# Kernel tuning notes

Hardware: AMD Instinct MI355X
Metric: run time of the kernel (lower is better)

## Reference

```python
import jax, jax.numpy as jnp
import numpy as np

N, F, E, T = 50000, 128, 800000, 8


def setup_inputs() -> dict:
    key = jax.random.key(0)
    ks = jax.random.split(key, 10)
    s = 1.0 / np.sqrt(F)
    return {
        "x": jax.random.normal(ks[0], (N, F), jnp.float32),
        "edge_index": jax.random.randint(ks[1], (2, E), 0, N, jnp.int64),
        "edge_weight": jax.random.uniform(ks[2], (E,), jnp.float32),
        "W0": jax.random.normal(ks[3], (F, F), jnp.float32) * s,
        "Wih": jax.random.normal(ks[4], (3 * F, F), jnp.float32) * s,
        "Whh": jax.random.normal(ks[5], (3 * F, F), jnp.float32) * s,
        "bih": jax.random.normal(ks[6], (3 * F,), jnp.float32) * s,
        "bhh": jax.random.normal(ks[7], (3 * F,), jnp.float32) * s,
        "Wlin": jax.random.normal(ks[8], (T, F), jnp.float32) * s,
        "blin": jax.random.normal(ks[9], (T,), jnp.float32) * s,
    }


def _evolve_weight(W0, Wih, Whh, bih, bhh):
    # One GRU step with input = hidden = W0 (rows of weight matrix as batch).
    gi = W0 @ Wih.T + bih  # [F, 3F]
    gh = W0 @ Whh.T + bhh
    ir, iz, inn = jnp.split(gi, 3, axis=1)
    hr, hz, hn = jnp.split(gh, 3, axis=1)
    r = jax.nn.sigmoid(ir + hr)
    z = jax.nn.sigmoid(iz + hz)
    n = jnp.tanh(inn + r * hn)
    return (1.0 - z) * n + z * W0  # [F, F]


def reference(x, edge_index, edge_weight, W0, Wih, Whh, bih, bhh, Wlin, blin):
    n_nodes = x.shape[0]
    W = _evolve_weight(W0, Wih, Whh, bih, bhh)
    # gcn_norm with added self-loops (fill value 1.0), symmetric normalization
    loop = jnp.arange(n_nodes, dtype=edge_index.dtype)
    row = jnp.concatenate([edge_index[0], loop])
    col = jnp.concatenate([edge_index[1], loop])
    ew = jnp.concatenate([edge_weight, jnp.ones((n_nodes,), edge_weight.dtype)])
    deg = jax.ops.segment_sum(ew, col, num_segments=n_nodes)
    dinv = jnp.where(deg > 0, jax.lax.rsqrt(jnp.where(deg > 0, deg, 1.0)), 0.0)
    norm = dinv[row] * ew * dinv[col]  # [E+N]
    xw = x @ W  # [N, F]
    h = jax.ops.segment_sum(norm[:, None] * xw[row], col, num_segments=n_nodes)
    h = jax.nn.relu(h)
    return h @ Wlin.T + blin  # [N, n_target]
```

## Files before the change

kernel.cpp:

```cpp
#include <hip/hip_runtime.h>
#include <math.h>

#define F 128
#define FIX18     262144.0f
#define INV18     (1.0f / 262144.0f)
#define EVB 256

using bf16x8 = __attribute__((ext_vector_type(8))) short;
using f32x4  = __attribute__((ext_vector_type(4))) float;

__device__ inline int read_idx(const int* ei, long long elem, int i64) {
    return i64 ? (int)((const long long*)ei)[elem] : ei[elem];
}
__device__ inline unsigned int f2bf_rn(float f) {
    unsigned int b = __float_as_uint(f);
    return (b + 0x7FFFu + ((b >> 16) & 1u)) >> 16;
}
__device__ inline float bflo(unsigned int u) { return __uint_as_float(u << 16); }
__device__ inline float bfhi(unsigned int u) { return __uint_as_float(u & 0xFFFF0000u); }

__device__ inline void acc8(float* acc, float wt, uint4 v) {
    acc[0] += wt * bflo(v.x); acc[1] += wt * bfhi(v.x);
    acc[2] += wt * bflo(v.y); acc[3] += wt * bfhi(v.y);
    acc[4] += wt * bflo(v.z); acc[5] += wt * bfhi(v.z);
    acc[6] += wt * bflo(v.w); acc[7] += wt * bfhi(v.w);
}

__device__ inline int detect_i64(const int* ei, int* sh) {
    if (threadIdx.x == 0) {
        int i64 = 1;
        for (int j = 0; j < 32; ++j) if (ei[2 * j + 1] != 0) { i64 = 0; break; }
        *sh = i64;
    }
    __syncthreads();
    return *sh;
}

__global__ __launch_bounds__(256) void k_count_evolve(
        const int* __restrict__ ei, const float* __restrict__ ew,
        unsigned int* __restrict__ packed8, int* __restrict__ pos,
        int E, int N,
        const float* __restrict__ W0, const float* __restrict__ Wih,
        const float* __restrict__ Whh, const float* __restrict__ bih,
        const float* __restrict__ bhh,
        unsigned short* __restrict__ Wth, unsigned short* __restrict__ Wtl) {
    __shared__ int i64sh;
    int wave = threadIdx.x >> 6, lane = threadIdx.x & 63;
    if ((int)blockIdx.x >= EVB) {
        int i64 = detect_i64(ei, &i64sh);
        int e = ((int)blockIdx.x - EVB) * 256 + threadIdx.x;
        if (e >= E) return;
        int c = read_idx(ei, (long long)E + e, i64);
        unsigned int copy = blockIdx.x & 7;
        unsigned int u = (1u << 24) | (unsigned int)(ew[e] * FIX18 + 0.5f);
        unsigned int old = atomicAdd(&packed8[(size_t)copy * N + c], u);
        pos[e] = (int)((old >> 24) | (copy << 24));
        return;
    }
    int gw = (int)blockIdx.x * 4 + wave;
    int pairBase = gw * 16;
    int i = pairBase >> 7;
    int jb = pairBase & 127;
    int lp = lane & 15, sl = lane >> 4;
    int j = jb + lp;
    const float* w0p = W0 + (size_t)i * F;
    const float* pir = Wih + (size_t)j * F;
    const float* piz = Wih + (size_t)(j + F) * F;
    const float* pin = Wih + (size_t)(j + 2 * F) * F;
    const float* phr = Whh + (size_t)j * F;
    const float* phz = Whh + (size_t)(j + F) * F;
    const float* phn = Whh + (size_t)(j + 2 * F) * F;
    float air = 0, aiz = 0, ain = 0, ahr = 0, ahz = 0, ahn = 0;
    int k0 = sl * 32;
    #pragma unroll
    for (int kk = 0; kk < 32; kk += 4) {
        int k = k0 + kk;
        float4 w0 = *(const float4*)&w0p[k];
        float4 a;
        a = *(const float4*)&pir[k]; air += w0.x*a.x + w0.y*a.y + w0.z*a.z + w0.w*a.w;
        a = *(const float4*)&piz[k]; aiz += w0.x*a.x + w0.y*a.y + w0.z*a.z + w0.w*a.w;
        a = *(const float4*)&pin[k]; ain += w0.x*a.x + w0.y*a.y + w0.z*a.z + w0.w*a.w;
        a = *(const float4*)&phr[k]; ahr += w0.x*a.x + w0.y*a.y + w0.z*a.z + w0.w*a.w;
        a = *(const float4*)&phz[k]; ahz += w0.x*a.x + w0.y*a.y + w0.z*a.z + w0.w*a.w;
        a = *(const float4*)&phn[k]; ahn += w0.x*a.x + w0.y*a.y + w0.z*a.z + w0.w*a.w;
    }
    air += __shfl_xor(air, 16, 64); air += __shfl_xor(air, 32, 64);
    aiz += __shfl_xor(aiz, 16, 64); aiz += __shfl_xor(aiz, 32, 64);
    ain += __shfl_xor(ain, 16, 64); ain += __shfl_xor(ain, 32, 64);
    ahr += __shfl_xor(ahr, 16, 64); ahr += __shfl_xor(ahr, 32, 64);
    ahz += __shfl_xor(ahz, 16, 64); ahz += __shfl_xor(ahz, 32, 64);
    ahn += __shfl_xor(ahn, 16, 64); ahn += __shfl_xor(ahn, 32, 64);
    if (sl == 0) {
        air += bih[j];          ahr += bhh[j];
        aiz += bih[j + F];      ahz += bhh[j + F];
        ain += bih[j + 2 * F];  ahn += bhh[j + 2 * F];
        float r = 1.0f / (1.0f + expf(-(air + ahr)));
        float z = 1.0f / (1.0f + expf(-(aiz + ahz)));
        float n = tanhf(ain + r * ahn);
        float w = (1.0f - z) * n + z * w0p[j];
        unsigned int hb = f2bf_rn(w);
        float whi = __uint_as_float(hb << 16);
        unsigned int lb = f2bf_rn(w - whi);
        Wth[j * F + i] = (unsigned short)hb;
        Wtl[j * F + i] = (unsigned short)lb;
    }
}

__global__ void k_bsum(const unsigned int* __restrict__ packed8,
                       int* __restrict__ bsum, int N) {
    __shared__ int s[4];
    int i = blockIdx.x * 256 + threadIdx.x;
    int v = 0;
    if (i < N) {
        #pragma unroll
        for (int k = 0; k < 8; ++k)
            v += (int)(packed8[(size_t)k * N + i] >> 24);
    }
    #pragma unroll
    for (int o = 1; o < 64; o <<= 1) v += __shfl_xor(v, o, 64);
    if ((threadIdx.x & 63) == 0) s[threadIdx.x >> 6] = v;
    __syncthreads();
    if (threadIdx.x == 0) bsum[blockIdx.x] = s[0] + s[1] + s[2] + s[3];
}

__global__ void k_offs(const unsigned int* __restrict__ packed8,
                       const int* __restrict__ bsum,
                       int* __restrict__ off, unsigned char* __restrict__ copyBase,
                       float* __restrict__ dinv, int N, int E, int nblk) {
    __shared__ int sdata[256];
    __shared__ int sred[4];
    __shared__ int sbase;
    int t = threadIdx.x;
    int b = blockIdx.x;
    int base = 0;
    for (int s0 = 0; s0 < nblk; s0 += 256) {
        int idx = s0 + t;
        int v = (idx < nblk && idx < b) ? bsum[idx] : 0;
        #pragma unroll
        for (int o = 1; o < 64; o <<= 1) v += __shfl_xor(v, o, 64);
        if ((t & 63) == 0) sred[t >> 6] = v;
        __syncthreads();
        if (t == 0) sbase = sred[0] + sred[1] + sred[2] + sred[3];
        __syncthreads();
        base += sbase;
        __syncthreads();
    }
    int i = b * 256 + t;
    int v = 0;
    unsigned int dsum = 0;
    if (i < N) {
        int run = 0;
        #pragma unroll
        for (int k = 0; k < 8; ++k) {
            unsigned int p = packed8[(size_t)k * N + i];
            copyBase[(size_t)i * 8 + k] = (unsigned char)run;
            run += (int)(p >> 24);
            dsum += (p & 0xFFFFFFu);
        }
        v = run;
    }
    sdata[t] = v;
    __syncthreads();
    #pragma unroll
    for (int s = 1; s < 256; s <<= 1) {
        int add = (t >= s) ? sdata[t - s] : 0;
        __syncthreads();
        sdata[t] += add;
        __syncthreads();
    }
    if (i < N) {
        off[i] = base + sdata[t] - v;
        dinv[i] = rsqrtf(1.0f + (float)dsum * INV18);
        if (i == N - 1) off[N] = E;
    }
}

__global__ __launch_bounds__(256) void k_place_cast(
        const int* __restrict__ ei, const float* __restrict__ ew,
        const int* __restrict__ off, const unsigned char* __restrict__ copyBase,
        const int* __restrict__ pos,
        int2* __restrict__ ep, int E, int placeBlocks,
        const float2* __restrict__ x2, const float* __restrict__ dinv,
        unsigned int* __restrict__ xs, int M) {
    __shared__ int i64sh;
    if ((int)blockIdx.x < placeBlocks) {
        int i64 = detect_i64(ei, &i64sh);
        int e = blockIdx.x * 256 + threadIdx.x;
        if (e >= E) return;
        int r = read_idx(ei, e, i64);
        int c = read_idx(ei, (long long)E + e, i64);
        unsigned int pe = (unsigned int)pos[e];
        int slot = off[c] + (int)copyBase[(size_t)c * 8 + (pe >> 24)] + (int)(pe & 0xFFFFFFu);
        ep[slot] = make_int2(r, __float_as_int(ew[e]));
    } else {
        int id = ((int)blockIdx.x - placeBlocks) * 256 + threadIdx.x;
        if (id >= M) return;
        float di = dinv[id >> 6];
        float2 v = x2[id];
        xs[id] = f2bf_rn(di * v.x) | (f2bf_rn(di * v.y) << 16);
    }
}

__global__ __launch_bounds__(256) void k_agg2(const uint4* __restrict__ xs4,
                                              const int* __restrict__ off,
                                              const int2* __restrict__ ep,
                                              const float* __restrict__ dinv,
                                              uint4* __restrict__ hagg4, int N) {
    int wave = threadIdx.x >> 6, lane = threadIdx.x & 63;
    int c = blockIdx.x * 4 + wave;
    if (c >= N) return;
    int g = lane >> 4, sl = lane & 15;
    int start = off[c], end = off[c + 1];
    float di = dinv[c];
    float a0[8] = {0,0,0,0,0,0,0,0}, a1[8] = {0,0,0,0,0,0,0,0};
    if (g == 0) {
        uint4 v = xs4[(size_t)c * 16 + sl];
        a0[0] = bflo(v.x); a0[1] = bfhi(v.x);
        a0[2] = bflo(v.y); a0[3] = bfhi(v.y);
        a0[4] = bflo(v.z); a0[5] = bfhi(v.z);
        a0[6] = bflo(v.w); a0[7] = bfhi(v.w);
    }
    int last = end - 1;
    for (int k = start; k < end; k += 16) {
        int iA = k + g, iB = k + g + 4, iC = k + g + 8, iD = k + g + 12;
        int2 eA = ep[min(iA, last)];
        int2 eB = ep[min(iB, last)];
        int2 eC = ep[min(iC, last)];
        int2 eD = ep[min(iD, last)];
        uint4 vA = xs4[(size_t)eA.x * 16 + sl];
        uint4 vB = xs4[(size_t)eB.x * 16 + sl];
        uint4 vC = xs4[(size_t)eC.x * 16 + sl];
        uint4 vD = xs4[(size_t)eD.x * 16 + sl];
        float wA = (iA <= last) ? __int_as_float(eA.y) : 0.f;
        float wB = (iB <= last) ? __int_as_float(eB.y) : 0.f;
        float wC = (iC <= last) ? __int_as_float(eC.y) : 0.f;
        float wD = (iD <= last) ? __int_as_float(eD.y) : 0.f;
        acc8(a0, wA, vA);
        acc8(a1, wB, vB);
        acc8(a0, wC, vC);
        acc8(a1, wD, vD);
    }
    #pragma unroll
    for (int f = 0; f < 8; ++f) {
        float v = a0[f] + a1[f];
        v += __shfl_xor(v, 16, 64);
        v += __shfl_xor(v, 32, 64);
        a0[f] = v;
    }
    if (lane < 16) {
        uint4 o;
        o.x = f2bf_rn(di * a0[0]) | (f2bf_rn(di * a0[1]) << 16);
        o.y = f2bf_rn(di * a0[2]) | (f2bf_rn(di * a0[3]) << 16);
        o.z = f2bf_rn(di * a0[4]) | (f2bf_rn(di * a0[5]) << 16);
        o.w = f2bf_rn(di * a0[6]) | (f2bf_rn(di * a0[7]) << 16);
        hagg4[(size_t)c * 16 + lane] = o;
    }
}

__global__ __launch_bounds__(256) void k_gemm(const uint4* __restrict__ hagg4,
                                              const unsigned short* __restrict__ Wth,
                                              const unsigned short* __restrict__ Wtl,
                                              const float* __restrict__ Wlin,
                                              const float* __restrict__ blin,
                                              float* __restrict__ out, int N) {
    __shared__ __align__(16) unsigned int At[64 * 68];
    __shared__ __align__(16) float WlinL[8 * F];
    int t = threadIdx.x;
    int row0 = blockIdx.x * 64;
    #pragma unroll
    for (int it = 0; it < 4; ++it) {
        int idx = it * 256 + t;
        int rr = idx >> 4, c4 = idx & 15;
        uint4 v = make_uint4(0u, 0u, 0u, 0u);
        if (row0 + rr < N) v = hagg4[(size_t)(row0 + rr) * 16 + c4];
        *(uint4*)&At[rr * 68 + c4 * 4] = v;
    }
    *(float4*)&WlinL[t * 4] = *(const float4*)&Wlin[t * 4];
    __syncthreads();

    int wave = t >> 6, lane = t & 63;
    int sl = lane & 15, q = lane >> 4;
    const unsigned short* Ash = (const unsigned short*)At;
    int mrow = wave * 16 + sl;

    f32x4 acc[8];
    #pragma unroll
    for (int nt = 0; nt < 8; ++nt) acc[nt] = (f32x4){0.f, 0.f, 0.f, 0.f};
    #pragma unroll
    for (int ko = 0; ko < 4; ++ko) {
        bf16x8 a = *(const bf16x8*)&Ash[mrow * 136 + ko * 32 + q * 8];
        #pragma unroll
        for (int nt = 0; nt < 8; ++nt) {
            int boff = (nt * 16 + sl) * F + ko * 32 + q * 8;
            bf16x8 bh = *(const bf16x8*)&Wth[boff];
            bf16x8 bl = *(const bf16x8*)&Wtl[boff];
            acc[nt] = __builtin_amdgcn_mfma_f32_16x16x32_bf16(a, bh, acc[nt], 0, 0, 0);
            acc[nt] = __builtin_amdgcn_mfma_f32_16x16x32_bf16(a, bl, acc[nt], 0, 0, 0);
        }
    }
    #pragma unroll
    for (int nt = 0; nt < 8; ++nt)
        #pragma unroll
        for (int r = 0; r < 4; ++r) acc[nt][r] = fmaxf(acc[nt][r], 0.f);

    float p[8][4];
    #pragma unroll
    for (int tt = 0; tt < 8; ++tt) {
        float wl[8];
        #pragma unroll
        for (int nt = 0; nt < 8; ++nt) wl[nt] = WlinL[tt * F + nt * 16 + sl];
        #pragma unroll
        for (int r = 0; r < 4; ++r) {
            float s = 0.f;
            #pragma unroll
            for (int nt = 0; nt < 8; ++nt) s += acc[nt][r] * wl[nt];
            p[tt][r] = s;
        }
    }
    #pragma unroll
    for (int tt = 0; tt < 8; ++tt)
        #pragma unroll
        for (int r = 0; r < 4; ++r) {
            float v = p[tt][r];
            v += __shfl_xor(v, 1, 64); v += __shfl_xor(v, 2, 64);
            v += __shfl_xor(v, 4, 64); v += __shfl_xor(v, 8, 64);
            p[tt][r] = v;
        }
    if (sl == 0) {
        #pragma unroll
        for (int r = 0; r < 4; ++r) {
            int row = row0 + wave * 16 + q * 4 + r;
            if (row < N) {
                #pragma unroll
                for (int tt = 0; tt < 8; ++tt)
                    out[(size_t)row * 8 + tt] = p[tt][r] + blin[tt];
            }
        }
    }
}

extern "C" void kernel_launch(void* const* d_in, const int* in_sizes, int n_in,
                              void* d_out, int out_size, void* d_ws, size_t ws_size,
                              hipStream_t stream) {
    const float* x    = (const float*)d_in[0];
    const int*   ei   = (const int*)d_in[1];
    const float* ew   = (const float*)d_in[2];
    const float* W0   = (const float*)d_in[3];
    const float* Wih  = (const float*)d_in[4];
    const float* Whh  = (const float*)d_in[5];
    const float* bih  = (const float*)d_in[6];
    const float* bhh  = (const float*)d_in[7];
    const float* Wlin = (const float*)d_in[8];
    const float* blin = (const float*)d_in[9];
    int N = in_sizes[0] / F;
    int E = in_sizes[1] / 2;
    float* outp = (float*)d_out;

    int nblk = (N + 255) / 256;
    int cntBlocks = (E + 255) / 256;
    int M = N * 64;

    char* wsb = (char*)d_ws;
    size_t cur = 0;
    auto alloc = [&](size_t sz) -> void* {
        void* p = wsb + cur;
        cur = (cur + sz + 255) & ~(size_t)255;
        return p;
    };
    unsigned int* packed8 = (unsigned int*)alloc((size_t)N * 8 * 4);
    float* dinv = (float*)alloc((size_t)N * 4);
    int*   off  = (int*)  alloc((size_t)(N + 1) * 4);
    int*   bsum = (int*)  alloc((size_t)nblk * 4);
    int*   pos  = (int*)  alloc((size_t)E * 4);
    unsigned char* copyBase = (unsigned char*)alloc((size_t)N * 8);
    int2*  ep   = (int2*) alloc((size_t)E * 8);
    unsigned short* Wth = (unsigned short*)alloc((size_t)F * F * 2);
    unsigned short* Wtl = (unsigned short*)alloc((size_t)F * F * 2);
    unsigned int* xs    = (unsigned int*)alloc((size_t)N * 64 * 4);
    unsigned int* hagg  = (unsigned int*)alloc((size_t)N * 64 * 4);
    (void)ws_size; (void)n_in; (void)out_size;

    hipMemsetAsync(packed8, 0, (size_t)N * 8 * 4, stream);
    hipLaunchKernelGGL(k_count_evolve, dim3(EVB + cntBlocks), dim3(256), 0, stream,
                       ei, ew, packed8, pos, E, N,
                       W0, Wih, Whh, bih, bhh, Wth, Wtl);
    hipLaunchKernelGGL(k_bsum, dim3(nblk), dim3(256), 0, stream, packed8, bsum, N);
    hipLaunchKernelGGL(k_offs, dim3(nblk), dim3(256), 0, stream,
                       packed8, bsum, off, copyBase, dinv, N, E, nblk);
    hipLaunchKernelGGL(k_place_cast, dim3(cntBlocks + (M + 255) / 256), dim3(256), 0, stream,
                       ei, ew, off, copyBase, pos, ep, E, cntBlocks,
                       (const float2*)x, dinv, xs, M);
    hipLaunchKernelGGL(k_agg2, dim3((N + 3) / 4), dim3(256), 0, stream,
                       (const uint4*)xs, off, ep, dinv, (uint4*)hagg, N);
    hipLaunchKernelGGL(k_gemm, dim3((N + 63) / 64), dim3(256), 0, stream,
                       (const uint4*)hagg, Wth, Wtl, Wlin, blin, outp, N);
}
```

Measured before the change: 212.5 us.

## Move x bf16 cast into count kernel; fold source dinv into edge weights

The unscaled bf16 cast of x now runs inside the first counting/evolve kernel instead of after the degree pass, so it no longer waits on dinv. The source-side normalization dinv[r] is folded into each edge weight at placement time, and the self-loop term is scaled by dinv in the aggregation. The per-edge position record shrinks from 32 to 16 bits, which assumes fewer than 256 edges per node per copy. That width limit could break correctness on skewed degree distributions, and the placement kernel now does an extra random dinv gather.

```diff
diff --git a/kernel.cpp b/kernel.cpp
--- a/kernel.cpp
+++ b/kernel.cpp
@@ -36,28 +36,37 @@
     return *sh;
 }
 
-__global__ __launch_bounds__(256) void k_count_evolve(
+__global__ __launch_bounds__(256) void k_count_evolve_cast(
         const int* __restrict__ ei, const float* __restrict__ ew,
-        unsigned int* __restrict__ packed8, int* __restrict__ pos,
-        int E, int N,
+        unsigned int* __restrict__ packed8, unsigned short* __restrict__ pos,
+        int E, int N, int cntBlocks,
         const float* __restrict__ W0, const float* __restrict__ Wih,
         const float* __restrict__ Whh, const float* __restrict__ bih,
         const float* __restrict__ bhh,
-        unsigned short* __restrict__ Wth, unsigned short* __restrict__ Wtl) {
+        unsigned short* __restrict__ Wth, unsigned short* __restrict__ Wtl,
+        const float2* __restrict__ x2, unsigned int* __restrict__ xs, int M) {
     __shared__ int i64sh;
-    int wave = threadIdx.x >> 6, lane = threadIdx.x & 63;
-    if ((int)blockIdx.x >= EVB) {
+    int b = (int)blockIdx.x;
+    if (b >= EVB + cntBlocks) {
+        int id = (b - EVB - cntBlocks) * 256 + threadIdx.x;
+        if (id >= M) return;
+        float2 v = x2[id];
+        xs[id] = f2bf_rn(v.x) | (f2bf_rn(v.y) << 16);
+        return;
+    }
+    if (b >= EVB) {
         int i64 = detect_i64(ei, &i64sh);
-        int e = ((int)blockIdx.x - EVB) * 256 + threadIdx.x;
+        int e = (b - EVB) * 256 + threadIdx.x;
         if (e >= E) return;
         int c = read_idx(ei, (long long)E + e, i64);
-        unsigned int copy = blockIdx.x & 7;
+        unsigned int copy = b & 7;
         unsigned int u = (1u << 24) | (unsigned int)(ew[e] * FIX18 + 0.5f);
         unsigned int old = atomicAdd(&packed8[(size_t)copy * N + c], u);
-        pos[e] = (int)((old >> 24) | (copy << 24));
+        pos[e] = (unsigned short)((old >> 24) | (copy << 8));
         return;
     }
-    int gw = (int)blockIdx.x * 4 + wave;
+    int wave = threadIdx.x >> 6, lane = threadIdx.x & 63;
+    int gw = b * 4 + wave;
     int pairBase = gw * 16;
     int i = pairBase >> 7;
     int jb = pairBase & 127;
@@ -175,30 +184,20 @@
     }
 }
 
-__global__ __launch_bounds__(256) void k_place_cast(
+__global__ __launch_bounds__(256) void k_place(
         const int* __restrict__ ei, const float* __restrict__ ew,
         const int* __restrict__ off, const unsigned char* __restrict__ copyBase,
-        const int* __restrict__ pos,
-        int2* __restrict__ ep, int E, int placeBlocks,
-        const float2* __restrict__ x2, const float* __restrict__ dinv,
-        unsigned int* __restrict__ xs, int M) {
+        const unsigned short* __restrict__ pos, const float* __restrict__ dinv,
+        int2* __restrict__ ep, int E) {
     __shared__ int i64sh;
-    if ((int)blockIdx.x < placeBlocks) {
-        int i64 = detect_i64(ei, &i64sh);
-        int e = blockIdx.x * 256 + threadIdx.x;
-        if (e >= E) return;
-        int r = read_idx(ei, e, i64);
-        int c = read_idx(ei, (long long)E + e, i64);
-        unsigned int pe = (unsigned int)pos[e];
-        int slot = off[c] + (int)copyBase[(size_t)c * 8 + (pe >> 24)] + (int)(pe & 0xFFFFFFu);
-        ep[slot] = make_int2(r, __float_as_int(ew[e]));
-    } else {
-        int id = ((int)blockIdx.x - placeBlocks) * 256 + threadIdx.x;
-        if (id >= M) return;
-        float di = dinv[id >> 6];
-        float2 v = x2[id];
-        xs[id] = f2bf_rn(di * v.x) | (f2bf_rn(di * v.y) << 16);
-    }
+    int i64 = detect_i64(ei, &i64sh);
+    int e = blockIdx.x * 256 + threadIdx.x;
+    if (e >= E) return;
+    int r = read_idx(ei, e, i64);
+    int c = read_idx(ei, (long long)E + e, i64);
+    unsigned int pe = (unsigned int)pos[e];
+    int slot = off[c] + (int)copyBase[(size_t)c * 8 + (pe >> 8)] + (int)(pe & 0xFFu);
+    ep[slot] = make_int2(r, __float_as_int(ew[e] * dinv[r]));
 }
 
 __global__ __launch_bounds__(256) void k_agg2(const uint4* __restrict__ xs4,
@@ -215,10 +214,7 @@
     float a0[8] = {0,0,0,0,0,0,0,0}, a1[8] = {0,0,0,0,0,0,0,0};
     if (g == 0) {
         uint4 v = xs4[(size_t)c * 16 + sl];
-        a0[0] = bflo(v.x); a0[1] = bfhi(v.x);
-        a0[2] = bflo(v.y); a0[3] = bfhi(v.y);
-        a0[4] = bflo(v.z); a0[5] = bfhi(v.z);
-        a0[6] = bflo(v.w); a0[7] = bfhi(v.w);
+        acc8(a0, di, v);
     }
     int last = end - 1;
     for (int k = start; k < end; k += 16) {
@@ -359,6 +355,7 @@
     int nblk = (N + 255) / 256;
     int cntBlocks = (E + 255) / 256;
     int M = N * 64;
+    int castBlocks = (M + 255) / 256;
 
     char* wsb = (char*)d_ws;
     size_t cur = 0;
@@ -371,7 +368,7 @@
     float* dinv = (float*)alloc((size_t)N * 4);
     int*   off  = (int*)  alloc((size_t)(N + 1) * 4);
     int*   bsum = (int*)  alloc((size_t)nblk * 4);
-    int*   pos  = (int*)  alloc((size_t)E * 4);
+    unsigned short* pos = (unsigned short*)alloc((size_t)E * 2);
     unsigned char* copyBase = (unsigned char*)alloc((size_t)N * 8);
     int2*  ep   = (int2*) alloc((size_t)E * 8);
     unsigned short* Wth = (unsigned short*)alloc((size_t)F * F * 2);
@@ -381,15 +378,15 @@
     (void)ws_size; (void)n_in; (void)out_size;
 
     hipMemsetAsync(packed8, 0, (size_t)N * 8 * 4, stream);
-    hipLaunchKernelGGL(k_count_evolve, dim3(EVB + cntBlocks), dim3(256), 0, stream,
-                       ei, ew, packed8, pos, E, N,
-                       W0, Wih, Whh, bih, bhh, Wth, Wtl);
+    hipLaunchKernelGGL(k_count_evolve_cast, dim3(EVB + cntBlocks + castBlocks), dim3(256), 0, stream,
+                       ei, ew, packed8, pos, E, N, cntBlocks,
+                       W0, Wih, Whh, bih, bhh, Wth, Wtl,
+                       (const float2*)x, xs, M);
     hipLaunchKernelGGL(k_bsum, dim3(nblk), dim3(256), 0, stream, packed8, bsum, N);
     hipLaunchKernelGGL(k_offs, dim3(nblk), dim3(256), 0, stream,
                        packed8, bsum, off, copyBase, dinv, N, E, nblk);
-    hipLaunchKernelGGL(k_place_cast, dim3(cntBlocks + (M + 255) / 256), dim3(256), 0, stream,
-                       ei, ew, off, copyBase, pos, ep, E, cntBlocks,
-                       (const float2*)x, dinv, xs, M);
+    hipLaunchKernelGGL(k_place, dim3(cntBlocks), dim3(256), 0, stream,
+                       ei, ew, off, copyBase, pos, dinv, ep, E);
     hipLaunchKernelGGL(k_agg2, dim3((N + 3) / 4), dim3(256), 0, stream,
                        (const uint4*)xs, off, ep, dinv, (uint4*)hagg, N);
     hipLaunchKernelGGL(k_gemm, dim3((N + 63) / 64), dim3(256), 0, stream,
```

Result: no change. 214.4 us (+0.9%).
